# Kernel tuning notes

Hardware: AMD Instinct MI355X
Metric: run time of the kernel (lower is better)

## Reference

```python
import jax, jax.numpy as jnp
import numpy as np

B, T, E = 2, 2048, 2048
H = 16
DH = E // H  # 128
FFN = 4 * E  # 8192
EPS = 1e-5


def _layernorm(x, g, b):
    mu = jnp.mean(x, axis=-1, keepdims=True)
    var = jnp.mean((x - mu) ** 2, axis=-1, keepdims=True)
    return (x - mu) * jax.lax.rsqrt(var + EPS) * g + b


def setup_inputs() -> dict:
    key = jax.random.key(0)
    ks = jax.random.split(key, 8)
    s = 0.02
    return {
        "x": jax.random.normal(ks[0], (B, T, E), jnp.float32),
        "g1": jnp.ones((E,), jnp.float32),
        "b1": jnp.zeros((E,), jnp.float32),
        "wq": jax.random.normal(ks[1], (E, E), jnp.float32) * s,
        "wk": jax.random.normal(ks[2], (E, E), jnp.float32) * s,
        "wv": jax.random.normal(ks[3], (E, E), jnp.float32) * s,
        "wo": jax.random.normal(ks[4], (E, E), jnp.float32) * s,
        "g2": jnp.ones((E,), jnp.float32),
        "b2": jnp.zeros((E,), jnp.float32),
        "w1": jax.random.normal(ks[5], (E, FFN), jnp.float32) * s,
        "w2": jax.random.normal(ks[6], (E, FFN), jnp.float32) * s,
        "w3": jax.random.normal(ks[7], (FFN, E), jnp.float32) * s,
    }


def reference(x, g1, b1, wq, wk, wv, wo, g2, b2, w1, w2, w3):
    Bx, Tx, Ex = x.shape
    # --- attention block (pre-LN, residual) ---
    h = _layernorm(x, g1, b1)
    q = (h @ wq).reshape(Bx, Tx, H, DH)
    k = (h @ wk).reshape(Bx, Tx, H, DH)
    v = (h @ wv).reshape(Bx, Tx, H, DH)
    scores = jnp.einsum('bqhd,bkhd->bhqk', q, k) / jnp.sqrt(jnp.float32(DH))
    causal = jnp.tril(jnp.ones((Tx, Tx), bool))  # [T,T]
    scores = jnp.where(causal[None, None], scores, -jnp.inf)
    attn = jax.nn.softmax(scores, axis=-1)
    ctx = jnp.einsum('bhqk,bkhd->bqhd', attn, v).reshape(Bx, Tx, H * DH)
    x = x + ctx @ wo
    # --- SwiGLU MLP block (pre-LN, residual) ---
    h = _layernorm(x, g2, b2)
    gated = jax.nn.silu(h @ w1) * (h @ w2)
    return x + gated @ w3
```

## Files before the change

kernel.cpp:

```cpp
#include <hip/hip_runtime.h>


#define T_SEQ 2048
#define E_DIM 2048
#define N_HEAD 16
#define D_HEAD 128
#define FFN_DIM 8192
#define M_ROWS 4096
#define QS (3 * E_DIM)

typedef unsigned short u16;
typedef short short8 __attribute__((ext_vector_type(8)));
typedef float f32x4 __attribute__((ext_vector_type(4)));

#define DEV __device__ __forceinline__

DEV u16 f2bf(float f) {
  unsigned u = __float_as_uint(f);
  u += 0x7fffu + ((u >> 16) & 1u);
  return (u16)(u >> 16);
}
DEV float bf2f(u16 h) { return __uint_as_float(((unsigned)h) << 16); }

DEV void async16(void* lds, const void* g) {
  __builtin_amdgcn_global_load_lds((const __attribute__((address_space(1))) void*)g,
                                   (__attribute__((address_space(3))) void*)lds, 16, 0, 0);
}

__global__ __launch_bounds__(256) void ln_kernel(const float* __restrict__ x,
                                                 const float* __restrict__ gw,
                                                 const float* __restrict__ bw,
                                                 u16* __restrict__ out) {
  int row = blockIdx.x;
  int t = threadIdx.x;
  const float4* xr = (const float4*)(x + (size_t)row * E_DIM);
  float4 a = xr[t], c = xr[t + 256];
  float s = a.x + a.y + a.z + a.w + c.x + c.y + c.z + c.w;
  float q = a.x * a.x + a.y * a.y + a.z * a.z + a.w * a.w +
            c.x * c.x + c.y * c.y + c.z * c.z + c.w * c.w;
  for (int off = 32; off > 0; off >>= 1) {
    s += __shfl_down(s, off);
    q += __shfl_down(q, off);
  }
  __shared__ float red[8];
  if ((t & 63) == 0) { red[(t >> 6) * 2] = s; red[(t >> 6) * 2 + 1] = q; }
  __syncthreads();
  s = red[0] + red[2] + red[4] + red[6];
  q = red[1] + red[3] + red[5] + red[7];
  float mu = s * (1.f / E_DIM);
  float rs = rsqrtf(q * (1.f / E_DIM) - mu * mu + 1e-5f);
  const float4* g4 = (const float4*)gw;
  const float4* b4 = (const float4*)bw;
  float4 g0 = g4[t], g1v = g4[t + 256], e0 = b4[t], e1 = b4[t + 256];
  ushort4 o0, o1;
  o0.x = f2bf((a.x - mu) * rs * g0.x + e0.x);
  o0.y = f2bf((a.y - mu) * rs * g0.y + e0.y);
  o0.z = f2bf((a.z - mu) * rs * g0.z + e0.z);
  o0.w = f2bf((a.w - mu) * rs * g0.w + e0.w);
  o1.x = f2bf((c.x - mu) * rs * g1v.x + e1.x);
  o1.y = f2bf((c.y - mu) * rs * g1v.y + e1.y);
  o1.z = f2bf((c.z - mu) * rs * g1v.z + e1.z);
  o1.w = f2bf((c.w - mu) * rs * g1v.w + e1.w);
  ((ushort4*)(out + (size_t)row * E_DIM))[t] = o0;
  ((ushort4*)(out + (size_t)row * E_DIM))[t + 256] = o1;
}

__global__ __launch_bounds__(256) void cvt_t_kernel(const float* __restrict__ W,
                                                    u16* __restrict__ WT,
                                                    int Kd, int Nd) {
  __shared__ float tile[32][33];
  int tx = threadIdx.x, ty = threadIdx.y;
  int n0 = blockIdx.x * 32, k0 = blockIdx.y * 32;
#pragma unroll
  for (int i = 0; i < 4; i++)
    tile[ty + i * 8][tx] = W[(size_t)(k0 + ty + i * 8) * Nd + n0 + tx];
  __syncthreads();
#pragma unroll
  for (int i = 0; i < 4; i++)
    WT[(size_t)(n0 + ty + i * 8) * Kd + k0 + tx] = f2bf(tile[tx][ty + i * 8]);
}

__global__ __launch_bounds__(256) void transpose_v_kernel(const u16* __restrict__ qkv,
                                                          u16* __restrict__ vt) {
  __shared__ u16 tile[32][33];
  int tx = threadIdx.x, ty = threadIdx.y;
  int b = blockIdx.z;
  int t0 = blockIdx.x * 32, e0 = blockIdx.y * 32;
#pragma unroll
  for (int i = 0; i < 4; i++)
    tile[ty + i * 8][tx] =
        qkv[(size_t)(b * T_SEQ + t0 + ty + i * 8) * QS + 2 * E_DIM + e0 + tx];
  __syncthreads();
#pragma unroll
  for (int i = 0; i < 4; i++)
    vt[((size_t)b * E_DIM + e0 + ty + i * 8) * T_SEQ + t0 + tx] = tile[tx][ty + i * 8];
}

__global__ __launch_bounds__(256) void add3_kernel(float* __restrict__ out,
                                                   const float* __restrict__ pk) {
  const size_t MN4 = (size_t)M_ROWS * E_DIM / 4;
  size_t i = (size_t)blockIdx.x * 256 + threadIdx.x;
  const float4* p04 = (const float4*)pk;
  const float4* p14 = (const float4*)(pk + (size_t)M_ROWS * E_DIM);
  float4* o4 = (float4*)out;
#pragma unroll
  for (int k = 0; k < 4; k++) {
    size_t idx = i + (size_t)k * 524288;
    if (idx < MN4) {
      float4 o = o4[idx], a = p04[idx], b = p14[idx];
      o.x += a.x + b.x; o.y += a.y + b.y;
      o.z += a.z + b.z; o.w += a.w + b.w;
      o4[idx] = o;
    }
  }
}

template <int MODE, int BM_>
__global__ __launch_bounds__(512, 1) void gemm8p(const u16* __restrict__ A,
                                                 const u16* __restrict__ BT,
                                                 void* __restrict__ Cout,
                                                 const void* __restrict__ Extra,
                                                 int N, int K, int lda, int ldb,
                                                 int CX, int CY) {
  constexpr int MM = BM_ / 64;
  constexpr int AUNIT = BM_ * 32;
  __shared__ u16 Abuf[4 * AUNIT];
  __shared__ u16 Bbuf[4 * 8192];
  const int t = threadIdx.x;
  const int w = t >> 6, l = t & 63, g = l >> 4, lq = l & 15;
  const int wm = w >> 2, wn = w & 3;

  const int bid = (blockIdx.z * gridDim.y + blockIdx.y) * gridDim.x + blockIdx.x;
  const int xcd = bid & 7, slot = bid >> 3;
  const int nchx = gridDim.x / CX;
  const int nchy = gridDim.y / CY;
  const int cpz = nchx * nchy;
  const int kz = xcd / cpz;
  const int cid = xcd % cpz;
  const int bx = (cid % nchx) * CX + (slot % CX);
  const int by = (cid / nchx) * CY + (slot / CX);
  const size_t bm = (size_t)by * BM_, bn = (size_t)bx * 256;
  const size_t koff = (size_t)kz * K;

  const int srcrow = ((l >> 3) << 1) | (l & 1);
  const int csrc = ((((l >> 1) & 3) ^ ((l >> 3) & 3)) << 3);
  const u16* aSrc = A + (bm + w * 16 + srcrow) * (size_t)lda + koff + csrc;
  const u16* bSrc = BT + (bn + w * 16 + srcrow) * (size_t)ldb + koff + csrc;
  const int rdoff = (((lq & 1) + 2 * (g ^ ((lq >> 1) & 3))) << 3);

#define STA8(DB, KS, TILE)                                                    \
  {                                                                           \
    u16* Ad = Abuf + (DB) * (2 * AUNIT) + (KS)*AUNIT + w * 512;               \
    const u16* as_ = aSrc + (size_t)(TILE)*64 + (KS)*32;                      \
    async16(Ad, as_);                                                         \
    if constexpr (BM_ == 256) async16(Ad + 4096, as_ + (size_t)128 * lda);    \
  }
#define STB8(DB, KS, TILE)                                                    \
  {                                                                           \
    u16* Bd = Bbuf + (DB)*16384 + (KS)*8192 + w * 512;                        \
    const u16* bs_ = bSrc + (size_t)(TILE)*64 + (KS)*32;                      \
    async16(Bd, bs_);                                                         \
    async16(Bd + 4096, bs_ + (size_t)128 * ldb);                              \
  }
#define RDA8(DB, KS, MH)                                                      \
  _Pragma("unroll") for (int mm = 0; mm < MM; ++mm)                           \
      af[mm] = *(const short8*)(Abuf + (DB) * (2 * AUNIT) + (KS)*AUNIT +      \
                                (wm * (BM_ / 4) + (MH) * (BM_ / 8) + mm * 8 + \
                                 (lq >> 1)) * 64 + rdoff);
#define RDB8(DB, KS)                                                          \
  _Pragma("unroll") for (int nn = 0; nn < 4; ++nn)                            \
      bf[nn] = *(const short8*)(Bbuf + (DB)*16384 + (KS)*8192 +               \
                                (wn * 32 + nn * 8 + (lq >> 1)) * 64 + rdoff);
#define MM168(MH)                                                             \
  _Pragma("unroll") for (int mm = 0; mm < MM; ++mm)                           \
      _Pragma("unroll") for (int nn = 0; nn < 4; ++nn)                        \
          acc[(MH)*MM + mm][nn] = __builtin_amdgcn_mfma_f32_16x16x32_bf16(    \
              af[mm], bf[nn], acc[(MH)*MM + mm][nn], 0, 0, 0);
#define SYNCA                                                                 \
  __builtin_amdgcn_s_barrier();                                               \
  asm volatile("s_waitcnt lgkmcnt(0)" ::: "memory");                          \
  __builtin_amdgcn_sched_barrier(0);                                          \
  __builtin_amdgcn_s_setprio(1);
#define ENDP __builtin_amdgcn_s_setprio(0);
#define BAR2 __builtin_amdgcn_s_barrier();
#define WAITN                                                                 \
  if constexpr (BM_ == 256) asm volatile("s_waitcnt vmcnt(8)" ::: "memory");  \
  else                      asm volatile("s_waitcnt vmcnt(6)" ::: "memory");
#define WAITH                                                                 \
  if constexpr (BM_ == 256) asm volatile("s_waitcnt vmcnt(4)" ::: "memory");  \
  else                      asm volatile("s_waitcnt vmcnt(3)" ::: "memory");

  const int NT = K >> 6, NI = NT >> 1;
  f32x4 acc[2 * MM][4] = {};
  short8 af[MM > 4 ? MM : 4], bf[4];

  STA8(0, 0, 0); STB8(0, 0, 0);
  STA8(0, 1, 0); STB8(0, 1, 0);
  STA8(1, 0, 1); STB8(1, 0, 1);
  WAITN;
  BAR2;

  for (int j = 0; j < NI; ++j) {
    const int t1 = 2 * j + 1, t2 = 2 * j + 2, t3 = 2 * j + 3;
    const bool s2 = t2 < NT, s3 = t3 < NT, lastI = (j + 1 == NI);
    RDB8(0, 0); RDA8(0, 0, 0);
    STA8(1, 1, t1);
    SYNCA; MM168(0); ENDP; BAR2;
    RDA8(0, 0, 1);
    STB8(1, 1, t1);
    SYNCA; MM168(1); ENDP;
    WAITN;
    BAR2;
    RDB8(0, 1); RDA8(0, 1, 0);
    if (s2) STA8(0, 0, t2);
    SYNCA; MM168(0); ENDP; BAR2;
    RDA8(0, 1, 1);
    if (s2) STB8(0, 0, t2);
    SYNCA; MM168(1); ENDP;
    if (lastI) { WAITH; } else { WAITN; }
    BAR2;
    RDB8(1, 0); RDA8(1, 0, 0);
    if (s2) STA8(0, 1, t2);
    SYNCA; MM168(0); ENDP; BAR2;
    RDA8(1, 0, 1);
    if (s2) STB8(0, 1, t2);
    SYNCA; MM168(1); ENDP;
    if (lastI) { asm volatile("s_waitcnt vmcnt(0)" ::: "memory"); } else { WAITN; }
    BAR2;
    RDB8(1, 1); RDA8(1, 1, 0);
    if (s3) STA8(1, 0, t3);
    SYNCA; MM168(0); ENDP; BAR2;
    RDA8(1, 1, 1);
    if (s3) STB8(1, 0, t3);
    SYNCA; MM168(1); ENDP;
    if (!lastI) { WAITN; }
    BAR2;
  }
#undef STA8
#undef STB8
#undef RDA8
#undef RDB8
#undef MM168
#undef SYNCA
#undef ENDP
#undef BAR2
#undef WAITN
#undef WAITH

  const size_t mn = (size_t)gridDim.y * BM_ * (size_t)N;
#pragma unroll
  for (int m = 0; m < 2 * MM; m++) {
    size_t row = bm + wm * (BM_ / 2) + m * 16 + 4 * g;
#pragma unroll
    for (int n = 0; n < 4; n++) {
      size_t col = bn + wn * 64 + n * 16 + lq;
#pragma unroll
      for (int r = 0; r < 4; r++) {
        size_t idx = (row + r) * (size_t)N + col;
        if constexpr (MODE == 0) {
          ((u16*)Cout)[idx] = f2bf(acc[m][n][r]);
        } else if constexpr (MODE == 1) {
          ((float*)Cout)[idx] = ((const float*)Extra)[idx] + acc[m][n][r];
        } else if constexpr (MODE == 2) {
          float a = bf2f(((const u16*)Extra)[idx]);
          float sil = a / (1.f + exp2f(-1.4426950408889634f * a));
          ((u16*)Cout)[idx] = f2bf(sil * acc[m][n][r]);
        } else {
          ((float*)Cout)[(size_t)kz * mn + idx] = acc[m][n][r];
        }
      }
    }
  }
}

__global__ __launch_bounds__(256, 2) void attn_kernel(const u16* __restrict__ QKV,
                                                      const u16* __restrict__ VT,
                                                      u16* __restrict__ CTX) {
  __shared__ u16 Ks[64 * 128];
  __shared__ u16 Vs[128 * 64];
  __shared__ u16 P_all[4][32 * 72];
  const int t = threadIdx.x;
  const int w = t >> 6, l = t & 63, g = l >> 4, lq = l & 15;
  u16* P = P_all[w];
  const int q0blk = blockIdx.x * 128;
  const int q0w = q0blk + w * 32;
  const int bh = blockIdx.y, b = bh >> 4, h = bh & 15;
  const u16* qp = QKV + (size_t)b * T_SEQ * QS + h * D_HEAD;
  const u16* kp = QKV + (size_t)b * T_SEQ * QS + E_DIM + h * D_HEAD;
  const u16* vp = VT + ((size_t)b * E_DIM + h * D_HEAD) * T_SEQ;

  short8 qf[2][4];
#pragma unroll
  for (int rg = 0; rg < 2; rg++)
#pragma unroll
    for (int ks = 0; ks < 4; ks++)
      qf[rg][ks] =
          *(const short8*)(qp + (size_t)(q0w + rg * 16 + lq) * QS + ks * 32 + g * 8);

  f32x4 acc[2][8] = {};
  float m2[2][4], ls[2][4];
#pragma unroll
  for (int rg = 0; rg < 2; rg++)
#pragma unroll
    for (int r = 0; r < 4; r++) { m2[rg][r] = -1e30f; ls[rg][r] = 0.f; }
  const float sc = 0.08838834764831845f * 1.4426950408889634f;

  const int kRow0 = 16 * w + (l >> 4);
  const int kChunk = l & 15;
  const int vRow0 = 32 * w + (l >> 3);
  const int vChunk = l & 7;

  for (int kv0 = 0; kv0 < q0blk + 128; kv0 += 64) {
#pragma unroll
    for (int j = 0; j < 4; j++) {
      int R = kRow0 + 4 * j;
      async16(Ks + (16 * w + 4 * j) * 128,
              kp + (size_t)(kv0 + R) * QS + ((kChunk ^ (R & 7)) << 3));
    }
#pragma unroll
    for (int j = 0; j < 4; j++) {
      int D = vRow0 + 8 * j;
      async16(Vs + (32 * w + 8 * j) * 64,
              vp + (size_t)D * T_SEQ + kv0 + ((vChunk ^ (D & 7)) << 3));
    }
    __syncthreads();

#pragma unroll
    for (int rg = 0; rg < 2; rg++) {
      const int rb = q0w + rg * 16;
      if (kv0 > rb + 15) continue;
      f32x4 s[4];
      __builtin_amdgcn_s_setprio(1);
#pragma unroll
      for (int ct = 0; ct < 4; ct++) {
        s[ct] = f32x4{0.f, 0.f, 0.f, 0.f};
#pragma unroll
        for (int ks = 0; ks < 4; ks++) {
          short8 kf = *(const short8*)(Ks + (ct * 16 + lq) * 128 +
                                       (((ks * 4 + g) ^ (lq & 7)) << 3));
          s[ct] = __builtin_amdgcn_mfma_f32_16x16x32_bf16(qf[rg][ks], kf, s[ct], 0, 0, 0);
        }
      }
      __builtin_amdgcn_s_setprio(0);
      float sv[4][4];
#pragma unroll
      for (int ct = 0; ct < 4; ct++)
#pragma unroll
        for (int r = 0; r < 4; r++) sv[ct][r] = s[ct][r] * sc;
      if (kv0 + 64 > rb) {
#pragma unroll
        for (int ct = 0; ct < 4; ct++)
#pragma unroll
          for (int r = 0; r < 4; r++)
            if (kv0 + ct * 16 + lq > rb + 4 * g + r) sv[ct][r] = -1e30f;
      }
      float mx[4];
#pragma unroll
      for (int r = 0; r < 4; r++)
        mx[r] = fmaxf(fmaxf(sv[0][r], sv[1][r]), fmaxf(sv[2][r], sv[3][r]));
#pragma unroll
      for (int off = 1; off < 16; off <<= 1)
#pragma unroll
        for (int r = 0; r < 4; r++) mx[r] = fmaxf(mx[r], __shfl_xor(mx[r], off));
#pragma unroll
      for (int r = 0; r < 4; r++) {
        float mn = fmaxf(m2[rg][r], mx[r]);
        float sca = exp2f(m2[rg][r] - mn);
        m2[rg][r] = mn;
        float sum = 0.f;
#pragma unroll
        for (int ct = 0; ct < 4; ct++) {
          float pv = exp2f(sv[ct][r] - mn);
          sum += pv;
          P[(rg * 16 + 4 * g + r) * 72 + ct * 16 + lq] = f2bf(pv);
        }
        ls[rg][r] = ls[rg][r] * sca + sum;
#pragma unroll
        for (int n = 0; n < 8; n++) acc[rg][n][r] *= sca;
      }
      short8 pa[2];
#pragma unroll
      for (int ks2 = 0; ks2 < 2; ks2++)
        pa[ks2] = *(const short8*)(P + (rg * 16 + lq) * 72 + ks2 * 32 + g * 8);
      __builtin_amdgcn_s_setprio(1);
#pragma unroll
      for (int n = 0; n < 8; n++)
#pragma unroll
        for (int ks2 = 0; ks2 < 2; ks2++) {
          short8 vf = *(const short8*)(Vs + (n * 16 + lq) * 64 +
                                       (((ks2 * 4 + g) ^ (lq & 7)) << 3));
          acc[rg][n] = __builtin_amdgcn_mfma_f32_16x16x32_bf16(pa[ks2], vf, acc[rg][n], 0, 0, 0);
        }
      __builtin_amdgcn_s_setprio(0);
    }
    __syncthreads();
  }

#pragma unroll
  for (int rg = 0; rg < 2; rg++) {
#pragma unroll
    for (int off = 1; off < 16; off <<= 1)
#pragma unroll
      for (int r = 0; r < 4; r++) ls[rg][r] += __shfl_xor(ls[rg][r], off);
  }
  u16* cp = CTX + ((size_t)b * T_SEQ + q0w) * E_DIM + h * D_HEAD;
#pragma unroll
  for (int rg = 0; rg < 2; rg++) {
    float inv[4];
#pragma unroll
    for (int r = 0; r < 4; r++) inv[r] = 1.f / ls[rg][r];
#pragma unroll
    for (int n = 0; n < 8; n++)
#pragma unroll
      for (int r = 0; r < 4; r++)
        cp[(size_t)(rg * 16 + 4 * g + r) * E_DIM + n * 16 + lq] =
            f2bf(acc[rg][n][r] * inv[r]);
  }
}

extern "C" void kernel_launch(void* const* d_in, const int* in_sizes, int n_in,
                              void* d_out, int out_size, void* d_ws, size_t ws_size,
                              hipStream_t stream) {
  (void)in_sizes; (void)n_in; (void)out_size; (void)ws_size;
  const float* x  = (const float*)d_in[0];
  const float* g1 = (const float*)d_in[1];
  const float* b1 = (const float*)d_in[2];
  const float* wq = (const float*)d_in[3];
  const float* wk = (const float*)d_in[4];
  const float* wv = (const float*)d_in[5];
  const float* wo = (const float*)d_in[6];
  const float* g2 = (const float*)d_in[7];
  const float* b2 = (const float*)d_in[8];
  const float* w1 = (const float*)d_in[9];
  const float* w2 = (const float*)d_in[10];
  const float* w3 = (const float*)d_in[11];
  float* out = (float*)d_out;

  const size_t EE2 = (size_t)E_DIM * E_DIM * 2;
  const size_t EF2 = (size_t)E_DIM * FFN_DIM * 2;
  const size_t ME2 = (size_t)M_ROWS * E_DIM * 2;
  char* p = (char*)d_ws;
  u16* wqkvT = (u16*)p; p += 3 * EE2;
  u16* woT = (u16*)p; p += EE2;
  u16* w1T = (u16*)p; p += EF2;
  u16* w2T = (u16*)p; p += EF2;
  u16* w3T = (u16*)p; p += EF2;
  u16* Hb  = (u16*)p; p += ME2;
  u16* QKVb = (u16*)p; p += (size_t)M_ROWS * QS * 2;
  u16* VTb = (u16*)p; p += ME2;
  u16* CTXb = (u16*)p; p += ME2;
  u16* U1b = QKVb;
  float* Pk = (float*)wqkvT;

  dim3 blk32(32, 8);
  cvt_t_kernel<<<dim3(E_DIM / 32, E_DIM / 32), blk32, 0, stream>>>(wq, wqkvT, E_DIM, E_DIM);
  cvt_t_kernel<<<dim3(E_DIM / 32, E_DIM / 32), blk32, 0, stream>>>(wk, wqkvT + E_DIM * E_DIM, E_DIM, E_DIM);
  cvt_t_kernel<<<dim3(E_DIM / 32, E_DIM / 32), blk32, 0, stream>>>(wv, wqkvT + 2 * E_DIM * E_DIM, E_DIM, E_DIM);
  cvt_t_kernel<<<dim3(E_DIM / 32, E_DIM / 32), blk32, 0, stream>>>(wo, woT, E_DIM, E_DIM);
  cvt_t_kernel<<<dim3(FFN_DIM / 32, E_DIM / 32), blk32, 0, stream>>>(w1, w1T, E_DIM, FFN_DIM);
  cvt_t_kernel<<<dim3(FFN_DIM / 32, E_DIM / 32), blk32, 0, stream>>>(w2, w2T, E_DIM, FFN_DIM);
  cvt_t_kernel<<<dim3(E_DIM / 32, FFN_DIM / 32), blk32, 0, stream>>>(w3, w3T, FFN_DIM, E_DIM);

  ln_kernel<<<M_ROWS, 256, 0, stream>>>(x, g1, b1, Hb);
  gemm8p<0, 128><<<dim3(QS / 256, M_ROWS / 128), 512, 0, stream>>>(
      Hb, wqkvT, QKVb, nullptr, QS, E_DIM, E_DIM, E_DIM, 6, 16);
  transpose_v_kernel<<<dim3(T_SEQ / 32, E_DIM / 32, 2), blk32, 0, stream>>>(QKVb, VTb);
  attn_kernel<<<dim3(T_SEQ / 128, 2 * N_HEAD), 256, 0, stream>>>(QKVb, VTb, CTXb);
  gemm8p<1, 128><<<dim3(E_DIM / 256, M_ROWS / 128), 512, 0, stream>>>(
      CTXb, woT, out, x, E_DIM, E_DIM, E_DIM, E_DIM, 4, 8);

  ln_kernel<<<M_ROWS, 256, 0, stream>>>(out, g2, b2, Hb);
  gemm8p<0, 256><<<dim3(FFN_DIM / 256, M_ROWS / 256), 512, 0, stream>>>(
      Hb, w1T, U1b, nullptr, FFN_DIM, E_DIM, E_DIM, E_DIM, 8, 8);
  gemm8p<2, 256><<<dim3(FFN_DIM / 256, M_ROWS / 256), 512, 0, stream>>>(
      Hb, w2T, U1b, U1b, FFN_DIM, E_DIM, E_DIM, E_DIM, 8, 8);
  gemm8p<3, 256><<<dim3(E_DIM / 256, M_ROWS / 256, 2), 512, 0, stream>>>(
      U1b, w3T, Pk, nullptr, E_DIM, FFN_DIM / 2, FFN_DIM, FFN_DIM, 4, 8);
  add3_kernel<<<2048, 256, 0, stream>>>(out, Pk);
}
```

Baseline: 910.2 us.

## Add 8-phase ping-pong pipelined GEMM kernel for MLP projections

Adds a new 256x256-tile bf16 MFMA GEMM kernel (gemm8pp) and uses it for the three MLP GEMMs. The kernel splits each K step into eight phases that interleave LDS fragment reads, async global-to-LDS loads for later tiles and MFMA blocks. It uses explicit sched_barrier, setprio and vmcnt waits to overlap memory traffic with compute. The aim is to hide load latency in the large FFN GEMMs, which dominate runtime. The cost is much more intricate hand scheduling, with a risk of barrier or wait-count mistakes that would break correctness or stall the pipeline.

```diff
diff --git a/kernel.cpp b/kernel.cpp
--- a/kernel.cpp
+++ b/kernel.cpp
@@ -111,6 +111,159 @@
       o.x += a.x + b.x; o.y += a.y + b.y;
       o.z += a.z + b.z; o.w += a.w + b.w;
       o4[idx] = o;
+    }
+  }
+}
+
+template <int MODE>
+__global__ __launch_bounds__(512, 1) void gemm8pp(const u16* __restrict__ A,
+                                                  const u16* __restrict__ BT,
+                                                  void* __restrict__ Cout,
+                                                  const void* __restrict__ Extra,
+                                                  int N, int K, int lda, int ldb,
+                                                  int CX, int CY) {
+  constexpr int AUNIT = 8192;
+  __shared__ u16 Abuf[4 * AUNIT];
+  __shared__ u16 Bbuf[4 * AUNIT];
+  const int t = threadIdx.x;
+  const int w = t >> 6, l = t & 63, g = l >> 4, lq = l & 15;
+  const int wm = w >> 2, wn = w & 3;
+
+  const int bid = (blockIdx.z * gridDim.y + blockIdx.y) * gridDim.x + blockIdx.x;
+  const int xcd = bid & 7, slot = bid >> 3;
+  const int nchx = gridDim.x / CX;
+  const int nchy = gridDim.y / CY;
+  const int cpz = nchx * nchy;
+  const int kz = xcd / cpz;
+  const int cid = xcd % cpz;
+  const int bx = (cid % nchx) * CX + (slot % CX);
+  const int by = (cid / nchx) * CY + (slot / CX);
+  const size_t bm = (size_t)by * 256, bn = (size_t)bx * 256;
+  const size_t koff = (size_t)kz * K;
+
+  const int srcrow = ((l >> 3) << 1) | (l & 1);
+  const int csrc = ((((l >> 1) & 3) ^ ((l >> 3) & 3)) << 3);
+  const u16* aSrc = A + (bm + w * 16 + srcrow) * (size_t)lda + koff + csrc;
+  const u16* bSrc = BT + (bn + w * 16 + srcrow) * (size_t)ldb + koff + csrc;
+  const int rdoff = (((lq & 1) + 2 * (g ^ ((lq >> 1) & 3))) << 3);
+
+#define STA(DB, KS, TILE)                                                     \
+  {                                                                           \
+    u16* Ad = Abuf + (DB) * (2 * AUNIT) + (KS)*AUNIT + w * 512;               \
+    const u16* as_ = aSrc + (size_t)(TILE)*64 + (KS)*32;                      \
+    async16(Ad, as_);                                                         \
+    async16(Ad + 4096, as_ + (size_t)128 * lda);                              \
+  }
+#define STB(DB, KS, TILE)                                                     \
+  {                                                                           \
+    u16* Bd = Bbuf + (DB) * (2 * AUNIT) + (KS)*AUNIT + w * 512;               \
+    const u16* bs_ = bSrc + (size_t)(TILE)*64 + (KS)*32;                      \
+    async16(Bd, bs_);                                                         \
+    async16(Bd + 4096, bs_ + (size_t)128 * ldb);                              \
+  }
+#define RDA(DST, DB, KS, MH)                                                  \
+  _Pragma("unroll") for (int mm = 0; mm < 4; ++mm)                            \
+      DST[mm] = *(const short8*)(Abuf + (DB) * (2 * AUNIT) + (KS)*AUNIT +     \
+                                 (wm * 64 + (MH)*32 + mm * 8 + (lq >> 1)) *   \
+                                     64 + rdoff);
+#define RDB(DST, DB, KS)                                                      \
+  _Pragma("unroll") for (int nn = 0; nn < 4; ++nn)                            \
+      DST[nn] = *(const short8*)(Bbuf + (DB) * (2 * AUNIT) + (KS)*AUNIT +     \
+                                 (wn * 32 + nn * 8 + (lq >> 1)) * 64 + rdoff);
+#define MMA(AF, BF, MH)                                                       \
+  _Pragma("unroll") for (int mm = 0; mm < 4; ++mm)                            \
+      _Pragma("unroll") for (int nn = 0; nn < 4; ++nn)                        \
+          acc[(MH)*4 + mm][nn] = __builtin_amdgcn_mfma_f32_16x16x32_bf16(     \
+              AF[mm], BF[nn], acc[(MH)*4 + mm][nn], 0, 0, 0);
+#define PIN __builtin_amdgcn_sched_barrier(0);
+#define SP1 __builtin_amdgcn_s_setprio(1);
+#define PH_END(VN_STR)                                                        \
+  __builtin_amdgcn_s_setprio(0);                                              \
+  __builtin_amdgcn_sched_barrier(0);                                          \
+  asm volatile("s_waitcnt vmcnt(" VN_STR ")" ::: "memory");                   \
+  __builtin_amdgcn_s_barrier();
+#define PH_ENDN                                                               \
+  __builtin_amdgcn_s_setprio(0);                                              \
+  __builtin_amdgcn_sched_barrier(0);                                          \
+  __builtin_amdgcn_s_barrier();
+
+  const int NT = K >> 6, NI = NT >> 1;
+  f32x4 acc[8][4] = {};
+  short8 af0[4], af1[4], bf0[4], bf1[4];
+
+  STA(0, 0, 0); STB(0, 0, 0);
+  STA(0, 1, 0); STB(0, 1, 0);
+  STA(1, 0, 1); STB(1, 0, 1);
+  asm volatile("s_waitcnt vmcnt(8)" ::: "memory");
+  __builtin_amdgcn_s_barrier();
+  RDA(af0, 0, 0, 0); RDB(bf0, 0, 0);
+
+  for (int j = 0; j < NI; ++j) {
+    const int t1 = 2 * j + 1, t2 = 2 * j + 2, t3 = 2 * j + 3;
+    const bool s2 = t2 < NT, s3 = t3 < NT, li = (j + 1 == NI);
+    RDA(af1, 0, 0, 1);
+    STA(1, 1, t1);
+    PIN; SP1; MMA(af0, bf0, 0);
+    PH_END("6")
+    RDA(af0, 0, 1, 0); RDB(bf1, 0, 1);
+    STB(1, 1, t1);
+    PIN; SP1; MMA(af1, bf0, 1);
+    PH_END("6")
+    RDA(af1, 0, 1, 1);
+    if (s2) STA(0, 0, t2);
+    PIN; SP1; MMA(af0, bf1, 0);
+    if (li) { PH_END("4") } else { PH_END("6") }
+    RDA(af0, 1, 0, 0); RDB(bf0, 1, 0);
+    if (s2) STB(0, 0, t2);
+    PIN; SP1; MMA(af1, bf1, 1);
+    if (li) { PH_END("4") } else { PH_END("6") }
+    RDA(af1, 1, 0, 1);
+    if (s2) STA(0, 1, t2);
+    PIN; SP1; MMA(af0, bf0, 0);
+    if (li) { PH_END("0") } else { PH_END("6") }
+    RDA(af0, 1, 1, 0); RDB(bf1, 1, 1);
+    if (s2) STB(0, 1, t2);
+    PIN; SP1; MMA(af1, bf0, 1);
+    if (li) { PH_ENDN } else { PH_END("6") }
+    RDA(af1, 1, 1, 1);
+    if (s3) STA(1, 0, t3);
+    PIN; SP1; MMA(af0, bf1, 0);
+    if (li) { PH_ENDN } else { PH_END("6") }
+    if (!li) { RDA(af0, 0, 0, 0); RDB(bf0, 0, 0); }
+    if (s3) STB(1, 0, t3);
+    PIN; SP1; MMA(af1, bf1, 1);
+    if (li) { PH_ENDN } else { PH_END("6") }
+  }
+#undef STA
+#undef STB
+#undef RDA
+#undef RDB
+#undef MMA
+#undef PIN
+#undef SP1
+#undef PH_END
+#undef PH_ENDN
+
+  const size_t mn = (size_t)gridDim.y * 256 * (size_t)N;
+#pragma unroll
+  for (int m = 0; m < 8; m++) {
+    size_t row = bm + wm * 128 + m * 16 + 4 * g;
+#pragma unroll
+    for (int n = 0; n < 4; n++) {
+      size_t col = bn + wn * 64 + n * 16 + lq;
+#pragma unroll
+      for (int r = 0; r < 4; r++) {
+        size_t idx = (row + r) * (size_t)N + col;
+        if constexpr (MODE == 0) {
+          ((u16*)Cout)[idx] = f2bf(acc[m][n][r]);
+        } else if constexpr (MODE == 2) {
+          float a = bf2f(((const u16*)Extra)[idx]);
+          float sil = a / (1.f + exp2f(-1.4426950408889634f * a));
+          ((u16*)Cout)[idx] = f2bf(sil * acc[m][n][r]);
+        } else {
+          ((float*)Cout)[(size_t)kz * mn + idx] = acc[m][n][r];
+        }
+      }
     }
   }
 }
@@ -470,11 +623,11 @@
       CTXb, woT, out, x, E_DIM, E_DIM, E_DIM, E_DIM, 4, 8);
 
   ln_kernel<<<M_ROWS, 256, 0, stream>>>(out, g2, b2, Hb);
-  gemm8p<0, 256><<<dim3(FFN_DIM / 256, M_ROWS / 256), 512, 0, stream>>>(
+  gemm8pp<0><<<dim3(FFN_DIM / 256, M_ROWS / 256), 512, 0, stream>>>(
       Hb, w1T, U1b, nullptr, FFN_DIM, E_DIM, E_DIM, E_DIM, 8, 8);
-  gemm8p<2, 256><<<dim3(FFN_DIM / 256, M_ROWS / 256), 512, 0, stream>>>(
+  gemm8pp<2><<<dim3(FFN_DIM / 256, M_ROWS / 256), 512, 0, stream>>>(
       Hb, w2T, U1b, U1b, FFN_DIM, E_DIM, E_DIM, E_DIM, 8, 8);
-  gemm8p<3, 256><<<dim3(E_DIM / 256, M_ROWS / 256, 2), 512, 0, stream>>>(
+  gemm8pp<3><<<dim3(E_DIM / 256, M_ROWS / 256, 2), 512, 0, stream>>>(
       U1b, w3T, Pk, nullptr, E_DIM, FFN_DIM / 2, FFN_DIM, FFN_DIM, 4, 8);
   add3_kernel<<<2048, 256, 0, stream>>>(out, Pk);
 }
```

Measured after the change: 1.080 ms. +18.7%, slower.

## Store split-K partials in bf16 and use larger M tile for QKV GEMM

Applied to the files above, without the earlier changes.

The split-K partial sums of the final MLP GEMM are now written as bf16 instead of fp32. The add kernel reads them as 8-wide bf16 vectors and adds them into the fp32 residual output. This halves the traffic for writing and reading the partials, at the cost of rounding each partial to bf16. Separately, the QKV projection GEMM now uses a 256-row tile instead of 128, with the grid swizzle parameter adjusted, to improve operand reuse.

```diff
diff --git a/kernel.cpp b/kernel.cpp
--- a/kernel.cpp
+++ b/kernel.cpp
@@ -97,22 +97,22 @@
 }
 
 __global__ __launch_bounds__(256) void add3_kernel(float* __restrict__ out,
-                                                   const float* __restrict__ pk) {
-  const size_t MN4 = (size_t)M_ROWS * E_DIM / 4;
-  size_t i = (size_t)blockIdx.x * 256 + threadIdx.x;
-  const float4* p04 = (const float4*)pk;
-  const float4* p14 = (const float4*)(pk + (size_t)M_ROWS * E_DIM);
-  float4* o4 = (float4*)out;
-#pragma unroll
-  for (int k = 0; k < 4; k++) {
-    size_t idx = i + (size_t)k * 524288;
-    if (idx < MN4) {
-      float4 o = o4[idx], a = p04[idx], b = p14[idx];
-      o.x += a.x + b.x; o.y += a.y + b.y;
-      o.z += a.z + b.z; o.w += a.w + b.w;
-      o4[idx] = o;
-    }
-  }
+                                                   const u16* __restrict__ pk) {
+  const size_t MN = (size_t)M_ROWS * E_DIM;
+  size_t base = ((size_t)blockIdx.x * 256 + threadIdx.x) * 8;
+  short8 a = *(const short8*)(pk + base);
+  short8 b = *(const short8*)(pk + MN + base);
+  float4 o0 = *(float4*)(out + base), o1 = *(float4*)(out + base + 4);
+  o0.x += bf2f((u16)a[0]) + bf2f((u16)b[0]);
+  o0.y += bf2f((u16)a[1]) + bf2f((u16)b[1]);
+  o0.z += bf2f((u16)a[2]) + bf2f((u16)b[2]);
+  o0.w += bf2f((u16)a[3]) + bf2f((u16)b[3]);
+  o1.x += bf2f((u16)a[4]) + bf2f((u16)b[4]);
+  o1.y += bf2f((u16)a[5]) + bf2f((u16)b[5]);
+  o1.z += bf2f((u16)a[6]) + bf2f((u16)b[6]);
+  o1.w += bf2f((u16)a[7]) + bf2f((u16)b[7]);
+  *(float4*)(out + base) = o0;
+  *(float4*)(out + base + 4) = o1;
 }
 
 template <int MODE, int BM_>
@@ -266,7 +266,7 @@
           float sil = a / (1.f + exp2f(-1.4426950408889634f * a));
           ((u16*)Cout)[idx] = f2bf(sil * acc[m][n][r]);
         } else {
-          ((float*)Cout)[(size_t)kz * mn + idx] = acc[m][n][r];
+          ((u16*)Cout)[(size_t)kz * mn + idx] = f2bf(acc[m][n][r]);
         }
       }
     }
@@ -450,7 +450,7 @@
   u16* VTb = (u16*)p; p += ME2;
   u16* CTXb = (u16*)p; p += ME2;
   u16* U1b = QKVb;
-  float* Pk = (float*)wqkvT;
+  u16* Pk = wqkvT;
 
   dim3 blk32(32, 8);
   cvt_t_kernel<<<dim3(E_DIM / 32, E_DIM / 32), blk32, 0, stream>>>(wq, wqkvT, E_DIM, E_DIM);
@@ -462,8 +462,8 @@
   cvt_t_kernel<<<dim3(E_DIM / 32, FFN_DIM / 32), blk32, 0, stream>>>(w3, w3T, FFN_DIM, E_DIM);
 
   ln_kernel<<<M_ROWS, 256, 0, stream>>>(x, g1, b1, Hb);
-  gemm8p<0, 128><<<dim3(QS / 256, M_ROWS / 128), 512, 0, stream>>>(
-      Hb, wqkvT, QKVb, nullptr, QS, E_DIM, E_DIM, E_DIM, 6, 16);
+  gemm8p<0, 256><<<dim3(QS / 256, M_ROWS / 256), 512, 0, stream>>>(
+      Hb, wqkvT, QKVb, nullptr, QS, E_DIM, E_DIM, E_DIM, 6, 8);
   transpose_v_kernel<<<dim3(T_SEQ / 32, E_DIM / 32, 2), blk32, 0, stream>>>(QKVb, VTb);
   attn_kernel<<<dim3(T_SEQ / 128, 2 * N_HEAD), 256, 0, stream>>>(QKVb, VTb, CTXb);
   gemm8p<1, 128><<<dim3(E_DIM / 256, M_ROWS / 128), 512, 0, stream>>>(
@@ -476,5 +476,5 @@
       Hb, w2T, U1b, U1b, FFN_DIM, E_DIM, E_DIM, E_DIM, 8, 8);
   gemm8p<3, 256><<<dim3(E_DIM / 256, M_ROWS / 256, 2), 512, 0, stream>>>(
       U1b, w3T, Pk, nullptr, E_DIM, FFN_DIM / 2, FFN_DIM, FFN_DIM, 4, 8);
-  add3_kernel<<<2048, 256, 0, stream>>>(out, Pk);
-}
+  add3_kernel<<<4096, 256, 0, stream>>>(out, Pk);
+}
```

After: 893.3 us. Within noise of the previous version (-1.9%).
